# Optimization experiments

Measured on AMD Instinct MI355X. Metric: run time of the kernel, lower is better.

The kernel has to match this reference:

```python
import jax, jax.numpy as jnp
import numpy as np
from jax import lax

H = 32  # hidden size

def _lstm_layer(x, w_ih, w_hh):
    # x: [B, T, D]; w_ih: [4H, D]; w_hh: [4H, H]; no biases.
    B, T, _ = x.shape
    # Precompute input contributions for all timesteps (one big GEMM).
    xg = jnp.einsum('btd,gd->btg', x, w_ih)  # [B, T, 4H]
    h0 = jnp.zeros((B, H), x.dtype)
    c0 = jnp.zeros((B, H), x.dtype)

    def step(carry, xg_t):
        h, c = carry
        gates = xg_t + h @ w_hh.T  # [B, 4H]
        i, f, g, o = jnp.split(gates, 4, axis=-1)  # PyTorch gate order i,f,g,o
        i = jax.nn.sigmoid(i)
        f = jax.nn.sigmoid(f)
        g = jnp.tanh(g)
        o = jax.nn.sigmoid(o)
        c = f * c + i * g
        h = o * jnp.tanh(c)
        return (h, c), h

    _, hs = lax.scan(step, (h0, c0), jnp.swapaxes(xg, 0, 1))  # hs: [T, B, H]
    return jnp.swapaxes(hs, 0, 1)  # [B, T, H]

def setup_inputs() -> dict:
    key = jax.random.key(0)
    ks = jax.random.split(key, 7)
    B, T, D = 4096, 512, 28
    s = lambda *sh: 0.1  # small init scale for stability over long scans
    return {
        'x':     jax.random.normal(ks[0], (B, T, D), jnp.float32),
        'w_ih0': jax.random.normal(ks[1], (4 * H, D), jnp.float32) * 0.1,
        'w_hh0': jax.random.normal(ks[2], (4 * H, H), jnp.float32) * 0.1,
        'w_ih1': jax.random.normal(ks[3], (4 * H, H), jnp.float32) * 0.1,
        'w_hh1': jax.random.normal(ks[4], (4 * H, H), jnp.float32) * 0.1,
        'w_out': jax.random.normal(ks[5], (10, H), jnp.float32) * 0.1,
        'b_out': jax.random.normal(ks[6], (10,), jnp.float32) * 0.1,
    }

def reference(x, w_ih0, w_hh0, w_ih1, w_hh1, w_out, b_out):
    h1 = _lstm_layer(x, w_ih0, w_hh0)   # layer 0 output [B, T, H]
    # Dropout(0.8) between layers is identity in eval mode.
    h2 = _lstm_layer(h1, w_ih1, w_hh1)  # layer 1 output [B, T, H]
    last = h2[:, -1, :]                  # [B, H]
    return last @ w_out.T + b_out        # [B, 10]
```

## Files before the change

kernel.cpp:

```cpp
#include <hip/hip_runtime.h>
#include <hip/hip_bf16.h>


#define T_LEN 512
#define D_IN  28

typedef __attribute__((ext_vector_type(8))) short short8;
typedef __attribute__((ext_vector_type(4))) float f32x4;
typedef __attribute__((ext_vector_type(4))) unsigned int u32x4;

#define K_SIG 1.4426950408889634f
#define K_TANH 2.8853900817779268f

__device__ __forceinline__ void split_bf16(float x, short& hi, short& lo) {
  unsigned u = __float_as_uint(x);
  hi = (short)(u >> 16);
  float hf_ = __uint_as_float(u & 0xFFFF0000u);
  float lf = x - hf_;
  lo = (short)(__float_as_uint(lf) >> 16);
}

__device__ __forceinline__ unsigned pk_hi16(float f1, float f0) {
  return __builtin_amdgcn_perm(__float_as_uint(f1), __float_as_uint(f0),
                               0x07060302u);
}
__device__ __forceinline__ float trunc_bf(float f) {
  return __uint_as_float(__float_as_uint(f) & 0xFFFF0000u);
}

__device__ __forceinline__ void lds_barrier() {
  asm volatile("s_waitcnt lgkmcnt(0)\n\ts_barrier" ::: "memory");
}

__device__ __forceinline__ void load_wtile(const float* __restrict__ W, int ldk,
                                           int kval, int n, int lane,
                                           short8& hi, short8& lo) {
  int row = n * 16 + (lane & 15);
  int kb = (lane >> 4) * 8;
  const float* p = W + row * ldk + kb;
#pragma unroll
  for (int i = 0; i < 8; ++i) {
    float v = (kb + i < kval) ? p[i] : 0.0f;
    short h, l;
    split_bf16(v, h, l);
    hi[i] = h; lo[i] = l;
  }
}

#define MFMA(a, b, c) __builtin_amdgcn_mfma_f32_16x16x32_bf16(a, b, c, 0, 0, 0)

__device__ __forceinline__ void pack_xfrag(const float4& A0, const float4& A1,
                                           short8& xh, short8& xl) {
  u32x4 xhu, xlu;
  xhu[0] = pk_hi16(A0.y, A0.x);
  xhu[1] = pk_hi16(A0.w, A0.z);
  xhu[2] = pk_hi16(A1.y, A1.x);
  xhu[3] = pk_hi16(A1.w, A1.z);
  float l0 = A0.x - trunc_bf(A0.x), l1 = A0.y - trunc_bf(A0.y);
  float l2 = A0.z - trunc_bf(A0.z), l3 = A0.w - trunc_bf(A0.w);
  float l4 = A1.x - trunc_bf(A1.x), l5 = A1.y - trunc_bf(A1.y);
  float l6 = A1.z - trunc_bf(A1.z), l7 = A1.w - trunc_bf(A1.w);
  xlu[0] = pk_hi16(l1, l0);
  xlu[1] = pk_hi16(l3, l2);
  xlu[2] = pk_hi16(l5, l4);
  xlu[3] = pk_hi16(l7, l6);
  xh = __builtin_bit_cast(short8, xhu);
  xl = __builtin_bit_cast(short8, xlu);
}

__device__ __forceinline__ void xside_mfma(f32x4* xacc, short8 xh, short8 xl,
                                           const short8* Bh, const short8* Bl) {
#pragma unroll
  for (int tt = 0; tt < 4; ++tt) {
    f32x4 z = {0.f, 0.f, 0.f, 0.f};
    xacc[tt] = MFMA(xh, Bh[tt], z);
  }
#pragma unroll
  for (int tt = 0; tt < 4; ++tt) xacc[tt] = MFMA(xl, Bh[tt], xacc[tt]);
#pragma unroll
  for (int tt = 0; tt < 4; ++tt) xacc[tt] = MFMA(xh, Bl[tt], xacc[tt]);
}

__device__ __forceinline__ void cell_update(const f32x4* acc, float* c, float* h) {
  float ei[4], ef[4], eg[4], eo[4];
#pragma unroll
  for (int r = 0; r < 4; ++r) {
    ei[r] = __builtin_amdgcn_exp2f(acc[0][r] * -K_SIG);
    ef[r] = __builtin_amdgcn_exp2f(acc[1][r] * -K_SIG);
    eg[r] = __builtin_amdgcn_exp2f(acc[2][r] * K_TANH);
    eo[r] = __builtin_amdgcn_exp2f(acc[3][r] * -K_SIG);
  }
  float num[4], D[4];
#pragma unroll
  for (int r = 0; r < 4; ++r) {
    float pig = (1.0f + ei[r]) * (1.0f + eg[r]);
    num[r] = c[r] * pig + (eg[r] - 1.0f) * (1.0f + ef[r]);
    D[r] = pig * (1.0f + ef[r]);
  }
  float R01 = __builtin_amdgcn_rcpf(D[0] * D[1]);
  float R23 = __builtin_amdgcn_rcpf(D[2] * D[3]);
  float cn[4];
  cn[0] = num[0] * D[1] * R01;
  cn[1] = num[1] * D[0] * R01;
  cn[2] = num[2] * D[3] * R23;
  cn[3] = num[3] * D[2] * R23;
  float ec[4], E[4];
#pragma unroll
  for (int r = 0; r < 4; ++r) ec[r] = __builtin_amdgcn_exp2f(cn[r] * K_TANH);
#pragma unroll
  for (int r = 0; r < 4; ++r) E[r] = (1.0f + eo[r]) * (1.0f + ec[r]);
  float S01 = __builtin_amdgcn_rcpf(E[0] * E[1]);
  float S23 = __builtin_amdgcn_rcpf(E[2] * E[3]);
  c[0] = cn[0]; h[0] = (ec[0] - 1.0f) * E[1] * S01;
  c[1] = cn[1]; h[1] = (ec[1] - 1.0f) * E[0] * S01;
  c[2] = cn[2]; h[2] = (ec[2] - 1.0f) * E[3] * S23;
  c[3] = cn[3]; h[3] = (ec[3] - 1.0f) * E[2] * S23;
}

template <int P>
__device__ __forceinline__ void l1_half(
    float4& NA0, float4& NA1, const float* __restrict__ ld, f32x4* xacc,
    const short8* Wxh, const short8* Wxl, const short8* Whh_, const short8* Whl,
    short (*h1)[2][16][40], float* c, float* h,
    int lrow, int lgrp, int kb, int uu) {
  constexpr int Q = P ^ 1;
  short8 ph = *(const short8*)&h1[Q][0][lrow][kb];
  short8 pl = *(const short8*)&h1[Q][1][lrow][kb];

  short8 xh, xl;
  pack_xfrag(NA0, NA1, xh, xl);
  NA0 = *(const float4*)(ld);
  if (lgrp < 3) NA1 = *(const float4*)(ld + 4);

  f32x4 acc[4];
#pragma unroll
  for (int tt = 0; tt < 4; ++tt) acc[tt] = MFMA(ph, Whh_[tt], xacc[tt]);
#pragma unroll
  for (int tt = 0; tt < 4; ++tt) acc[tt] = MFMA(pl, Whh_[tt], acc[tt]);
#pragma unroll
  for (int tt = 0; tt < 4; ++tt) acc[tt] = MFMA(ph, Whl[tt], acc[tt]);

  cell_update(acc, c, h);
#pragma unroll
  for (int r = 0; r < 4; ++r) {
    short hh_, ll_;
    split_bf16(h[r], hh_, ll_);
    int row = lgrp * 4 + r;
    h1[P][0][row][uu] = hh_;
    h1[P][1][row][uu] = ll_;
  }

  xside_mfma(xacc, xh, xl, Wxh, Wxl);
}

template <int P>
__device__ __forceinline__ void l2_half(
    const short8* Wxh, const short8* Wxl, const short8* Whh_, const short8* Whl,
    short (*h1)[2][16][40], short (*h2)[2][16][40], float* c, float* h,
    int lrow, int lgrp, int kb, int uu, bool writeout) {
  constexpr int Q = P ^ 1;
  short8 ah = *(const short8*)&h1[Q][0][lrow][kb];
  short8 al = *(const short8*)&h1[Q][1][lrow][kb];
  short8 ph = *(const short8*)&h2[Q][0][lrow][kb];
  short8 pl = *(const short8*)&h2[Q][1][lrow][kb];
  f32x4 acc[4];
#pragma unroll
  for (int tt = 0; tt < 4; ++tt) {
    f32x4 z = {0.f, 0.f, 0.f, 0.f};
    acc[tt] = MFMA(ah, Wxh[tt], z);
  }
#pragma unroll
  for (int tt = 0; tt < 4; ++tt) acc[tt] = MFMA(al, Wxh[tt], acc[tt]);
#pragma unroll
  for (int tt = 0; tt < 4; ++tt) acc[tt] = MFMA(ah, Wxl[tt], acc[tt]);
#pragma unroll
  for (int tt = 0; tt < 4; ++tt) acc[tt] = MFMA(ph, Whh_[tt], acc[tt]);
#pragma unroll
  for (int tt = 0; tt < 4; ++tt) acc[tt] = MFMA(pl, Whh_[tt], acc[tt]);
#pragma unroll
  for (int tt = 0; tt < 4; ++tt) acc[tt] = MFMA(ph, Whl[tt], acc[tt]);

  cell_update(acc, c, h);
  if (writeout) {
#pragma unroll
    for (int r = 0; r < 4; ++r) {
      short hh_, ll_;
      split_bf16(h[r], hh_, ll_);
      int row = lgrp * 4 + r;
      h2[P][0][row][uu] = hh_;
      h2[P][1][row][uu] = ll_;
    }
  }
}

__global__ __launch_bounds__(256) void lstm2_pipe(
    const float* __restrict__ x, const float* __restrict__ wih0,
    const float* __restrict__ whh0, const float* __restrict__ wih1,
    const float* __restrict__ whh1, const float* __restrict__ wout,
    const float* __restrict__ bout, float* __restrict__ out) {
  __shared__ short h1buf[2][2][16][40];
  __shared__ short h2buf[2][2][16][40];
  __shared__ float hf[16][33];

  const int tid = threadIdx.x;
  const int lane = tid & 63;
  const int wid = tid >> 6;
  const int layer = wid >> 1;
  const int w01 = wid & 1;
  const int b0 = blockIdx.x * 16;

  for (int i = tid; i < 2 * 2 * 16 * 40; i += 256) {
    ((short*)h1buf)[i] = 0;
    ((short*)h2buf)[i] = 0;
  }

  const int lrow = lane & 15;
  const int lgrp = lane >> 4;
  const int kb = lgrp * 8;
  const int uu = lrow + 16 * w01;

  const float* Wih = layer ? wih1 : wih0;
  const float* Whh = layer ? whh1 : whh0;
  const int ldk = layer ? 32 : 28;

  short8 Wxh[4], Wxl[4], Whh_[4], Whl[4];
#pragma unroll
  for (int tt = 0; tt < 4; ++tt) {
    int n = tt * 2 + w01;
    load_wtile(Wih, ldk, ldk, n, lane, Wxh[tt], Wxl[tt]);
    load_wtile(Whh, 32, 32, n, lane, Whh_[tt], Whl[tt]);
  }

  float c[4] = {0, 0, 0, 0}, h[4] = {0, 0, 0, 0};

  const float* xrow = x + ((size_t)(b0 + lrow)) * T_LEN * D_IN + kb;

  float4 XOA0 = make_float4(0, 0, 0, 0), XOA1 = make_float4(0, 0, 0, 0);
  float4 XEA0 = make_float4(0, 0, 0, 0), XEA1 = make_float4(0, 0, 0, 0);
  f32x4 xacc[4];
  if (layer == 0) {
    float4 Z0 = *(const float4*)(xrow);
    float4 Z1 = make_float4(0, 0, 0, 0);
    if (lgrp < 3) Z1 = *(const float4*)(xrow + 4);
    XOA0 = *(const float4*)(xrow + D_IN);
    if (lgrp < 3) XOA1 = *(const float4*)(xrow + D_IN + 4);
    XEA0 = *(const float4*)(xrow + 2 * D_IN);
    if (lgrp < 3) XEA1 = *(const float4*)(xrow + 2 * D_IN + 4);
    short8 xh0, xl0;
    pack_xfrag(Z0, Z1, xh0, xl0);
    xside_mfma(xacc, xh0, xl0, Wxh, Wxl);
  }

  __syncthreads();

  for (int s = 0; s < T_LEN; s += 2) {
    {
      int t3 = s + 3 < T_LEN ? s + 3 : T_LEN - 1;
      const float* ld = xrow + (size_t)t3 * D_IN;
      if (layer == 0) {
        l1_half<0>(XOA0, XOA1, ld, xacc, Wxh, Wxl, Whh_, Whl, h1buf, c, h,
                   lrow, lgrp, kb, uu);
      } else if (s > 0) {
        l2_half<0>(Wxh, Wxl, Whh_, Whl, h1buf, h2buf, c, h,
                   lrow, lgrp, kb, uu, true);
      }
      lds_barrier();
    }
    {
      int t4 = s + 4 < T_LEN ? s + 4 : T_LEN - 1;
      const float* ld = xrow + (size_t)t4 * D_IN;
      if (layer == 0) {
        l1_half<1>(XEA0, XEA1, ld, xacc, Wxh, Wxl, Whh_, Whl, h1buf, c, h,
                   lrow, lgrp, kb, uu);
      } else {
        l2_half<1>(Wxh, Wxl, Whh_, Whl, h1buf, h2buf, c, h,
                   lrow, lgrp, kb, uu, true);
      }
      lds_barrier();
    }
  }

  if (layer == 1) {
    l2_half<0>(Wxh, Wxl, Whh_, Whl, h1buf, h2buf, c, h,
               lrow, lgrp, kb, uu, false);
#pragma unroll
    for (int r = 0; r < 4; ++r) hf[lgrp * 4 + r][uu] = h[r];
  }
  __syncthreads();

  for (int j = tid; j < 160; j += 256) {
    int row = j / 10, col = j % 10;
    float s = bout[col];
#pragma unroll
    for (int u = 0; u < 32; ++u) s += hf[row][u] * wout[col * 32 + u];
    out[(size_t)(b0 + row) * 10 + col] = s;
  }
}

extern "C" void kernel_launch(void* const* d_in, const int* in_sizes, int n_in,
                              void* d_out, int out_size, void* d_ws, size_t ws_size,
                              hipStream_t stream) {
  const float* x = (const float*)d_in[0];
  const float* wih0 = (const float*)d_in[1];
  const float* whh0 = (const float*)d_in[2];
  const float* wih1 = (const float*)d_in[3];
  const float* whh1 = (const float*)d_in[4];
  const float* wout = (const float*)d_in[5];
  const float* bout = (const float*)d_in[6];
  float* out = (float*)d_out;
  lstm2_pipe<<<256, 256, 0, stream>>>(x, wih0, whh0, wih1, whh1, wout, bout, out);
}
```

Before: 352.6 us.

## Deepen layer pipeline with 4-slot h1 ring and prefetched layer-2 inputs

Layer 1's input-side MFMAs move back onto the critical path of each step, in place of being precomputed one step ahead. Layer 2 now reads its h1 input one barrier earlier, lagging two steps behind through a 4-deep h1 ring buffer, so the LDS read latency is hidden behind the barrier. The loop is unrolled by four with extra drain iterations. This adds 12 MFMAs to layer 0's recurrent path, but aims to balance the two waves' latency and take LDS loads off layer 2's critical path.

```diff
diff --git a/kernel.cpp b/kernel.cpp
--- a/kernel.cpp
+++ b/kernel.cpp
@@ -68,19 +68,6 @@
   xl = __builtin_bit_cast(short8, xlu);
 }
 
-__device__ __forceinline__ void xside_mfma(f32x4* xacc, short8 xh, short8 xl,
-                                           const short8* Bh, const short8* Bl) {
-#pragma unroll
-  for (int tt = 0; tt < 4; ++tt) {
-    f32x4 z = {0.f, 0.f, 0.f, 0.f};
-    xacc[tt] = MFMA(xh, Bh[tt], z);
-  }
-#pragma unroll
-  for (int tt = 0; tt < 4; ++tt) xacc[tt] = MFMA(xl, Bh[tt], xacc[tt]);
-#pragma unroll
-  for (int tt = 0; tt < 4; ++tt) xacc[tt] = MFMA(xh, Bl[tt], xacc[tt]);
-}
-
 __device__ __forceinline__ void cell_update(const f32x4* acc, float* c, float* h) {
   float ei[4], ef[4], eg[4], eo[4];
 #pragma unroll
@@ -119,26 +106,35 @@
 
 template <int P>
 __device__ __forceinline__ void l1_half(
-    float4& NA0, float4& NA1, const float* __restrict__ ld, f32x4* xacc,
-    const short8* Wxh, const short8* Wxl, const short8* Whh_, const short8* Whl,
+    float4& A0, float4& A1, const float* __restrict__ ld,
+    const short8* WxH, const short8* WxL, const short8* WhH, const short8* WhL,
     short (*h1)[2][16][40], float* c, float* h,
     int lrow, int lgrp, int kb, int uu) {
-  constexpr int Q = P ^ 1;
+  constexpr int Q = (P + 3) & 3;
   short8 ph = *(const short8*)&h1[Q][0][lrow][kb];
   short8 pl = *(const short8*)&h1[Q][1][lrow][kb];
 
   short8 xh, xl;
-  pack_xfrag(NA0, NA1, xh, xl);
-  NA0 = *(const float4*)(ld);
-  if (lgrp < 3) NA1 = *(const float4*)(ld + 4);
+  pack_xfrag(A0, A1, xh, xl);
+  A0 = *(const float4*)(ld);
+  if (lgrp < 3) A1 = *(const float4*)(ld + 4);
 
   f32x4 acc[4];
 #pragma unroll
-  for (int tt = 0; tt < 4; ++tt) acc[tt] = MFMA(ph, Whh_[tt], xacc[tt]);
-#pragma unroll
-  for (int tt = 0; tt < 4; ++tt) acc[tt] = MFMA(pl, Whh_[tt], acc[tt]);
-#pragma unroll
-  for (int tt = 0; tt < 4; ++tt) acc[tt] = MFMA(ph, Whl[tt], acc[tt]);
+  for (int tt = 0; tt < 4; ++tt) {
+    f32x4 z = {0.f, 0.f, 0.f, 0.f};
+    acc[tt] = MFMA(xh, WxH[tt], z);
+  }
+#pragma unroll
+  for (int tt = 0; tt < 4; ++tt) acc[tt] = MFMA(xl, WxH[tt], acc[tt]);
+#pragma unroll
+  for (int tt = 0; tt < 4; ++tt) acc[tt] = MFMA(xh, WxL[tt], acc[tt]);
+#pragma unroll
+  for (int tt = 0; tt < 4; ++tt) acc[tt] = MFMA(ph, WhH[tt], acc[tt]);
+#pragma unroll
+  for (int tt = 0; tt < 4; ++tt) acc[tt] = MFMA(pl, WhH[tt], acc[tt]);
+#pragma unroll
+  for (int tt = 0; tt < 4; ++tt) acc[tt] = MFMA(ph, WhL[tt], acc[tt]);
 
   cell_update(acc, c, h);
 #pragma unroll
@@ -149,48 +145,46 @@
     h1[P][0][row][uu] = hh_;
     h1[P][1][row][uu] = ll_;
   }
-
-  xside_mfma(xacc, xh, xl, Wxh, Wxl);
 }
 
 template <int P>
 __device__ __forceinline__ void l2_half(
-    const short8* Wxh, const short8* Wxl, const short8* Whh_, const short8* Whl,
+    short8& a1h, short8& a1l,
+    const short8* WxH, const short8* WxL, const short8* WhH, const short8* WhL,
     short (*h1)[2][16][40], short (*h2)[2][16][40], float* c, float* h,
-    int lrow, int lgrp, int kb, int uu, bool writeout) {
-  constexpr int Q = P ^ 1;
-  short8 ah = *(const short8*)&h1[Q][0][lrow][kb];
-  short8 al = *(const short8*)&h1[Q][1][lrow][kb];
-  short8 ph = *(const short8*)&h2[Q][0][lrow][kb];
-  short8 pl = *(const short8*)&h2[Q][1][lrow][kb];
-  f32x4 acc[4];
-#pragma unroll
-  for (int tt = 0; tt < 4; ++tt) {
-    f32x4 z = {0.f, 0.f, 0.f, 0.f};
-    acc[tt] = MFMA(ah, Wxh[tt], z);
-  }
-#pragma unroll
-  for (int tt = 0; tt < 4; ++tt) acc[tt] = MFMA(al, Wxh[tt], acc[tt]);
-#pragma unroll
-  for (int tt = 0; tt < 4; ++tt) acc[tt] = MFMA(ah, Wxl[tt], acc[tt]);
-#pragma unroll
-  for (int tt = 0; tt < 4; ++tt) acc[tt] = MFMA(ph, Whh_[tt], acc[tt]);
-#pragma unroll
-  for (int tt = 0; tt < 4; ++tt) acc[tt] = MFMA(pl, Whh_[tt], acc[tt]);
-#pragma unroll
-  for (int tt = 0; tt < 4; ++tt) acc[tt] = MFMA(ph, Whl[tt], acc[tt]);
-
-  cell_update(acc, c, h);
-  if (writeout) {
+    int lrow, int lgrp, int kb, int uu, bool compute) {
+  if (compute) {
+    short8 p2h = *(const short8*)&h2[(P + 1) & 1][0][lrow][kb];
+    short8 p2l = *(const short8*)&h2[(P + 1) & 1][1][lrow][kb];
+    f32x4 acc[4];
+#pragma unroll
+    for (int tt = 0; tt < 4; ++tt) {
+      f32x4 z = {0.f, 0.f, 0.f, 0.f};
+      acc[tt] = MFMA(a1h, WxH[tt], z);
+    }
+#pragma unroll
+    for (int tt = 0; tt < 4; ++tt) acc[tt] = MFMA(a1l, WxH[tt], acc[tt]);
+#pragma unroll
+    for (int tt = 0; tt < 4; ++tt) acc[tt] = MFMA(a1h, WxL[tt], acc[tt]);
+#pragma unroll
+    for (int tt = 0; tt < 4; ++tt) acc[tt] = MFMA(p2h, WhH[tt], acc[tt]);
+#pragma unroll
+    for (int tt = 0; tt < 4; ++tt) acc[tt] = MFMA(p2l, WhH[tt], acc[tt]);
+#pragma unroll
+    for (int tt = 0; tt < 4; ++tt) acc[tt] = MFMA(p2h, WhL[tt], acc[tt]);
+
+    cell_update(acc, c, h);
 #pragma unroll
     for (int r = 0; r < 4; ++r) {
       short hh_, ll_;
       split_bf16(h[r], hh_, ll_);
       int row = lgrp * 4 + r;
-      h2[P][0][row][uu] = hh_;
-      h2[P][1][row][uu] = ll_;
-    }
-  }
+      h2[P & 1][0][row][uu] = hh_;
+      h2[P & 1][1][row][uu] = ll_;
+    }
+  }
+  a1h = *(const short8*)&h1[(P + 3) & 3][0][lrow][kb];
+  a1l = *(const short8*)&h1[(P + 3) & 3][1][lrow][kb];
 }
 
 __global__ __launch_bounds__(256) void lstm2_pipe(
@@ -198,7 +192,7 @@
     const float* __restrict__ whh0, const float* __restrict__ wih1,
     const float* __restrict__ whh1, const float* __restrict__ wout,
     const float* __restrict__ bout, float* __restrict__ out) {
-  __shared__ short h1buf[2][2][16][40];
+  __shared__ short h1buf[4][2][16][40];
   __shared__ short h2buf[2][2][16][40];
   __shared__ float hf[16][33];
 
@@ -209,10 +203,8 @@
   const int w01 = wid & 1;
   const int b0 = blockIdx.x * 16;
 
-  for (int i = tid; i < 2 * 2 * 16 * 40; i += 256) {
-    ((short*)h1buf)[i] = 0;
-    ((short*)h2buf)[i] = 0;
-  }
+  for (int i = tid; i < 4 * 2 * 16 * 40; i += 256) ((short*)h1buf)[i] = 0;
+  for (int i = tid; i < 2 * 2 * 16 * 40; i += 256) ((short*)h2buf)[i] = 0;
 
   const int lrow = lane & 15;
   const int lgrp = lane >> 4;
@@ -223,66 +215,81 @@
   const float* Whh = layer ? whh1 : whh0;
   const int ldk = layer ? 32 : 28;
 
-  short8 Wxh[4], Wxl[4], Whh_[4], Whl[4];
+  short8 WxH[4], WxL[4], WhH[4], WhL[4];
 #pragma unroll
   for (int tt = 0; tt < 4; ++tt) {
     int n = tt * 2 + w01;
-    load_wtile(Wih, ldk, ldk, n, lane, Wxh[tt], Wxl[tt]);
-    load_wtile(Whh, 32, 32, n, lane, Whh_[tt], Whl[tt]);
+    load_wtile(Wih, ldk, ldk, n, lane, WxH[tt], WxL[tt]);
+    load_wtile(Whh, 32, 32, n, lane, WhH[tt], WhL[tt]);
   }
 
   float c[4] = {0, 0, 0, 0}, h[4] = {0, 0, 0, 0};
 
   const float* xrow = x + ((size_t)(b0 + lrow)) * T_LEN * D_IN + kb;
 
-  float4 XOA0 = make_float4(0, 0, 0, 0), XOA1 = make_float4(0, 0, 0, 0);
-  float4 XEA0 = make_float4(0, 0, 0, 0), XEA1 = make_float4(0, 0, 0, 0);
-  f32x4 xacc[4];
+  float4 X0A0 = make_float4(0, 0, 0, 0), X0A1 = make_float4(0, 0, 0, 0);
+  float4 X1A0 = make_float4(0, 0, 0, 0), X1A1 = make_float4(0, 0, 0, 0);
   if (layer == 0) {
-    float4 Z0 = *(const float4*)(xrow);
-    float4 Z1 = make_float4(0, 0, 0, 0);
-    if (lgrp < 3) Z1 = *(const float4*)(xrow + 4);
-    XOA0 = *(const float4*)(xrow + D_IN);
-    if (lgrp < 3) XOA1 = *(const float4*)(xrow + D_IN + 4);
-    XEA0 = *(const float4*)(xrow + 2 * D_IN);
-    if (lgrp < 3) XEA1 = *(const float4*)(xrow + 2 * D_IN + 4);
-    short8 xh0, xl0;
-    pack_xfrag(Z0, Z1, xh0, xl0);
-    xside_mfma(xacc, xh0, xl0, Wxh, Wxl);
-  }
+    X0A0 = *(const float4*)(xrow);
+    if (lgrp < 3) X0A1 = *(const float4*)(xrow + 4);
+    X1A0 = *(const float4*)(xrow + D_IN);
+    if (lgrp < 3) X1A1 = *(const float4*)(xrow + D_IN + 4);
+  }
+
+  short8 a1h = {0, 0, 0, 0, 0, 0, 0, 0};
+  short8 a1l = a1h;
 
   __syncthreads();
 
-  for (int s = 0; s < T_LEN; s += 2) {
-    {
-      int t3 = s + 3 < T_LEN ? s + 3 : T_LEN - 1;
-      const float* ld = xrow + (size_t)t3 * D_IN;
-      if (layer == 0) {
-        l1_half<0>(XOA0, XOA1, ld, xacc, Wxh, Wxl, Whh_, Whl, h1buf, c, h,
-                   lrow, lgrp, kb, uu);
-      } else if (s > 0) {
-        l2_half<0>(Wxh, Wxl, Whh_, Whl, h1buf, h2buf, c, h,
-                   lrow, lgrp, kb, uu, true);
+#pragma unroll 1
+  for (int s = 0; s < 516; s += 4) {
+    if (layer == 0) {
+      if (s < T_LEN) {
+        int t = (s + 2 < T_LEN) ? s + 2 : T_LEN - 1;
+        l1_half<0>(X0A0, X0A1, xrow + (size_t)t * D_IN, WxH, WxL, WhH, WhL,
+                   h1buf, c, h, lrow, lgrp, kb, uu);
       }
-      lds_barrier();
-    }
-    {
-      int t4 = s + 4 < T_LEN ? s + 4 : T_LEN - 1;
-      const float* ld = xrow + (size_t)t4 * D_IN;
-      if (layer == 0) {
-        l1_half<1>(XEA0, XEA1, ld, xacc, Wxh, Wxl, Whh_, Whl, h1buf, c, h,
-                   lrow, lgrp, kb, uu);
-      } else {
-        l2_half<1>(Wxh, Wxl, Whh_, Whl, h1buf, h2buf, c, h,
-                   lrow, lgrp, kb, uu, true);
+    } else {
+      l2_half<0>(a1h, a1l, WxH, WxL, WhH, WhL, h1buf, h2buf, c, h,
+                 lrow, lgrp, kb, uu, (s >= 2) && (s < T_LEN + 2));
+    }
+    lds_barrier();
+    if (layer == 0) {
+      if (s + 1 < T_LEN) {
+        int t = (s + 3 < T_LEN) ? s + 3 : T_LEN - 1;
+        l1_half<1>(X1A0, X1A1, xrow + (size_t)t * D_IN, WxH, WxL, WhH, WhL,
+                   h1buf, c, h, lrow, lgrp, kb, uu);
       }
-      lds_barrier();
-    }
+    } else {
+      l2_half<1>(a1h, a1l, WxH, WxL, WhH, WhL, h1buf, h2buf, c, h,
+                 lrow, lgrp, kb, uu, (s + 1 >= 2) && (s + 1 < T_LEN + 2));
+    }
+    lds_barrier();
+    if (layer == 0) {
+      if (s + 2 < T_LEN) {
+        int t = (s + 4 < T_LEN) ? s + 4 : T_LEN - 1;
+        l1_half<2>(X0A0, X0A1, xrow + (size_t)t * D_IN, WxH, WxL, WhH, WhL,
+                   h1buf, c, h, lrow, lgrp, kb, uu);
+      }
+    } else {
+      l2_half<2>(a1h, a1l, WxH, WxL, WhH, WhL, h1buf, h2buf, c, h,
+                 lrow, lgrp, kb, uu, (s + 2 >= 2) && (s + 2 < T_LEN + 2));
+    }
+    lds_barrier();
+    if (layer == 0) {
+      if (s + 3 < T_LEN) {
+        int t = (s + 5 < T_LEN) ? s + 5 : T_LEN - 1;
+        l1_half<3>(X1A0, X1A1, xrow + (size_t)t * D_IN, WxH, WxL, WhH, WhL,
+                   h1buf, c, h, lrow, lgrp, kb, uu);
+      }
+    } else {
+      l2_half<3>(a1h, a1l, WxH, WxL, WhH, WhL, h1buf, h2buf, c, h,
+                 lrow, lgrp, kb, uu, (s + 3 >= 2) && (s + 3 < T_LEN + 2));
+    }
+    lds_barrier();
   }
 
   if (layer == 1) {
-    l2_half<0>(Wxh, Wxl, Whh_, Whl, h1buf, h2buf, c, h,
-               lrow, lgrp, kb, uu, false);
 #pragma unroll
     for (int r = 0; r < 4; ++r) hf[lgrp * 4 + r][uu] = h[r];
   }
```

Result: faster. 324.0 us (-8.1%).
